# Performance work log

Hardware: AMD Instinct MI355X
Metric: run time of the kernel (lower is better)

The kernel has to match this reference:

```python
import jax, jax.numpy as jnp
import numpy as np

TOP_K = 2  # top-k experts per token


def setup_inputs() -> dict:
    key = jax.random.key(0)
    k1, k2, k3, k4, k5 = jax.random.split(key, 5)
    B, S, D = 1, 2048, 2048
    E, F = 8, 1408
    scale = 0.02
    return {
        "hidden_states": jax.random.normal(k1, (B, S, D), dtype=jnp.float32),
        "gate_w": jax.random.normal(k2, (E, D), dtype=jnp.float32) * scale,
        "w_gate": jax.random.normal(k3, (E, D, F), dtype=jnp.float32) * scale,
        "w_up": jax.random.normal(k4, (E, D, F), dtype=jnp.float32) * scale,
        "w_down": jax.random.normal(k5, (E, F, D), dtype=jnp.float32) * scale,
    }


def reference(hidden_states, gate_w, w_gate, w_up, w_down):
    B, S, D = hidden_states.shape
    T = B * S
    x = hidden_states.reshape(T, D)  # flatten tokens, as in forward()

    # Router: combined gate built from per-rank 1-row gates -> [T, E] logits
    router_logits = jnp.einsum("td,ed->te", x, gate_w)
    routing_weights = jax.nn.softmax(router_logits, axis=-1)
    top_w, top_idx = jax.lax.top_k(routing_weights, TOP_K)  # [T, K]

    # Per-token combine weight for each expert (0 if expert not selected).
    # Equivalent to the one_hot expert_mask + index_add combine in the module.
    comb = jnp.zeros((T, gate_w.shape[0]), dtype=routing_weights.dtype)
    comb = comb.at[jnp.arange(T)[:, None], top_idx].add(top_w)  # [T, E]

    # Each expert is a Qwen2 MLP: down(silu(gate(x)) * up(x)).
    # (Dispatch/all-to-all collapses to dense-per-expert + masked combine
    #  on a single device; tokens with comb==0 contribute nothing.)
    g = jnp.einsum("td,edf->etf", x, w_gate)
    u = jnp.einsum("td,edf->etf", x, w_up)
    y = jnp.einsum("etf,efd->etd", jax.nn.silu(g) * u, w_down)  # [E, T, D]

    out = jnp.einsum("te,etd->td", comb, y)  # weighted combine (index_add)
    return out.reshape(B, S, D)
```

## Files before the change

### kernel.cpp

```cpp
#include <hip/hip_runtime.h>
#include <stdint.h>


#define TT 2048
#define DD 2048
#define FF 1408
#define NE 8
#define HROWS 5120
#define TRASH (2*TT)

typedef float f32x4 __attribute__((ext_vector_type(4)));
typedef short bf16x8 __attribute__((ext_vector_type(8)));

__device__ __forceinline__ unsigned short f2bf(float f) {
    unsigned int x = __float_as_uint(f);
    return (unsigned short)((x + 0x7fffu + ((x >> 16) & 1u)) >> 16);
}
__device__ __forceinline__ float bf2f(unsigned short u) {
    union { unsigned int i; float f; } v; v.i = ((unsigned int)u) << 16; return v.f;
}
__device__ __forceinline__ uint4 cvt8(float4 a, float4 b) {
    uint4 o; unsigned short* po = (unsigned short*)&o;
    po[0] = f2bf(a.x); po[1] = f2bf(a.y); po[2] = f2bf(a.z); po[3] = f2bf(a.w);
    po[4] = f2bf(b.x); po[5] = f2bf(b.y); po[6] = f2bf(b.z); po[7] = f2bf(b.w);
    return o;
}

__device__ __forceinline__ void transpose_tile(const float* __restrict__ src,
                                               unsigned short* __restrict__ dst,
                                               int R, int C, int r0, int c0) {
    __shared__ unsigned short tile[64][65];
    const int tid = threadIdx.x;
    const int lr = tid >> 3;
    const int lc = (tid & 7) * 8;
#pragma unroll
    for (int p = 0; p < 2; ++p) {
        int rr = lr + p * 32;
        const float* sp = &src[(size_t)(r0 + rr) * C + c0 + lc];
        float4 a = ((const float4*)sp)[0];
        float4 b = ((const float4*)sp)[1];
        uint4 v = cvt8(a, b);
        const unsigned short* pv = (const unsigned short*)&v;
#pragma unroll
        for (int i = 0; i < 8; ++i) tile[rr][lc + i] = pv[i];
    }
    __syncthreads();
#pragma unroll
    for (int p = 0; p < 2; ++p) {
        int cc = lr + p * 32;
        uint4 o; unsigned short* po = (unsigned short*)&o;
#pragma unroll
        for (int i = 0; i < 8; ++i) po[i] = tile[lc + i][cc];
        *(uint4*)&dst[(size_t)(c0 + cc) * R + r0 + lc] = o;
    }
}

__global__ void transpose_gu_kernel(const float* __restrict__ wg,
                                    const float* __restrict__ wu,
                                    unsigned short* __restrict__ WgT,
                                    unsigned short* __restrict__ WuT) {
    const int z = blockIdx.z;
    const float* src; unsigned short* dst;
    if (z < 8) { src = wg + (size_t)z * DD * FF;       dst = WgT + (size_t)z * FF * DD; }
    else       { src = wu + (size_t)(z - 8) * DD * FF; dst = WuT + (size_t)(z - 8) * FF * DD; }
    transpose_tile(src, dst, DD, FF, blockIdx.y * 64, blockIdx.x * 64);
}

__global__ void transpose_d_kernel(const float* __restrict__ wd,
                                   unsigned short* __restrict__ WdT) {
    const int z = blockIdx.z;
    transpose_tile(wd + (size_t)z * FF * DD, WdT + (size_t)z * DD * FF,
                   FF, DD, blockIdx.y * 64, blockIdx.x * 64);
}

__global__ void router_kernel(const float* __restrict__ x,
                              const float* __restrict__ gw,
                              int* __restrict__ cnt,
                              int* __restrict__ tok,
                              float* __restrict__ wtv,
                              int* __restrict__ dstv) {
    const int wv = threadIdx.x >> 6, lane = threadIdx.x & 63;
    const int t = blockIdx.x * 4 + wv;
    float acc[NE];
#pragma unroll
    for (int e = 0; e < NE; ++e) acc[e] = 0.f;
    const float* xr = x + (size_t)t * DD;
    for (int j = lane; j < DD; j += 64) {
        float xv = xr[j];
#pragma unroll
        for (int e = 0; e < NE; ++e) acc[e] += xv * gw[e * DD + j];
    }
#pragma unroll
    for (int e = 0; e < NE; ++e) {
        float v = acc[e];
        v += __shfl_xor(v, 32); v += __shfl_xor(v, 16); v += __shfl_xor(v, 8);
        v += __shfl_xor(v, 4);  v += __shfl_xor(v, 2);  v += __shfl_xor(v, 1);
        acc[e] = v;
    }
    if (lane == 0) {
        float mx = acc[0];
#pragma unroll
        for (int e = 1; e < NE; ++e) mx = fmaxf(mx, acc[e]);
        float p[NE], s = 0.f;
#pragma unroll
        for (int e = 0; e < NE; ++e) { p[e] = __expf(acc[e] - mx); s += p[e]; }
        int i0 = 0;
#pragma unroll
        for (int e = 1; e < NE; ++e) if (p[e] > p[i0]) i0 = e;
        int i1 = (i0 == 0) ? 1 : 0;
#pragma unroll
        for (int e = 0; e < NE; ++e) if (e != i0 && p[e] > p[i1]) i1 = e;
        float inv = 1.f / s;
        int p0 = atomicAdd(&cnt[i0], 1);
        tok[i0 * TT + p0] = t; wtv[i0 * TT + p0] = p[i0] * inv; dstv[i0 * TT + p0] = 2 * t;
        int p1 = atomicAdd(&cnt[i1], 1);
        tok[i1 * TT + p1] = t; wtv[i1 * TT + p1] = p[i1] * inv; dstv[i1 * TT + p1] = 2 * t + 1;
    }
}

__global__ void finalize_kernel(const int* __restrict__ cnt,
                                int* __restrict__ base,
                                int* __restrict__ cntpad,
                                int* __restrict__ tok,
                                float* __restrict__ wtv,
                                int* __restrict__ dstv) {
    __shared__ int sc[NE], sp[NE];
    if (threadIdx.x == 0) {
        int b = 0;
        for (int e = 0; e < NE; ++e) {
            int c = cnt[e]; int pd = (c + 127) & ~127;
            base[e] = b; cntpad[e] = pd; sc[e] = c; sp[e] = pd; b += pd;
        }
    }
    __syncthreads();
    for (int e = 0; e < NE; ++e)
        for (int i = sc[e] + (int)threadIdx.x; i < sp[e]; i += 256) {
            tok[e * TT + i] = 0; wtv[e * TT + i] = 0.f; dstv[e * TT + i] = TRASH;
        }
}

__launch_bounds__(256, 2)
__global__ void gemm1_kernel(const float* __restrict__ x,
                             const unsigned short* __restrict__ WgT,
                             const unsigned short* __restrict__ WuT,
                             const int* __restrict__ tok,
                             const int* __restrict__ base,
                             const int* __restrict__ cntpad,
                             unsigned short* __restrict__ H) {
    __shared__ unsigned short As[128 * 32];
    __shared__ unsigned short Bg[128 * 32];
    __shared__ unsigned short Bu[128 * 32];
    __shared__ int s_tok[128];

    const int e = blockIdx.z, rb = blockIdx.y, fb = blockIdx.x;
    const int cp = cntpad[e];
    if (rb * 128 >= cp) return;
    const int b0 = base[e];

    const int tid = threadIdx.x;
    if (tid < 128) s_tok[tid] = tok[e * TT + rb * 128 + tid];
    __syncthreads();

    const int w = tid >> 6, lane = tid & 63;
    const int r = lane & 15, q = lane >> 4;
    const int wm = w & 1, wn = w >> 1;

    const int srow = w * 32 + (lane >> 2);
    const int koff = (lane & 3) * 8;
    const float* ga0 = x + (size_t)s_tok[srow] * DD + koff;
    const float* ga1 = x + (size_t)s_tok[srow + 16] * DD + koff;
    const size_t wb = (size_t)e * FF * DD + (size_t)(fb * 128 + srow) * DD + koff;
    const unsigned short* gg0 = WgT + wb;
    const unsigned short* gg1 = WgT + wb + (size_t)16 * DD;
    const unsigned short* gu0 = WuT + wb;
    const unsigned short* gu1 = WuT + wb + (size_t)16 * DD;
    uint4* sa0 = (uint4*)&As[srow * 32 + koff];  uint4* sa1 = (uint4*)&As[(srow + 16) * 32 + koff];
    uint4* sg0 = (uint4*)&Bg[srow * 32 + koff];  uint4* sg1 = (uint4*)&Bg[(srow + 16) * 32 + koff];
    uint4* su0 = (uint4*)&Bu[srow * 32 + koff];  uint4* su1 = (uint4*)&Bu[(srow + 16) * 32 + koff];

    f32x4 accg[4][4] = {};
    f32x4 accu[4][4] = {};

    for (int kt = 0; kt < DD / 32; ++kt) {
        uint4 va0 = cvt8(((const float4*)ga0)[0], ((const float4*)ga0)[1]);
        uint4 va1 = cvt8(((const float4*)ga1)[0], ((const float4*)ga1)[1]);
        uint4 vg0 = *(const uint4*)gg0;  uint4 vg1 = *(const uint4*)gg1;
        uint4 vu0 = *(const uint4*)gu0;  uint4 vu1 = *(const uint4*)gu1;
        ga0 += 32; ga1 += 32; gg0 += 32; gg1 += 32; gu0 += 32; gu1 += 32;
        __syncthreads();
        *sa0 = va0; *sa1 = va1; *sg0 = vg0; *sg1 = vg1; *su0 = vu0; *su1 = vu1;
        __syncthreads();
        bf16x8 af[4], gf[4], uf[4];
#pragma unroll
        for (int m = 0; m < 4; ++m)
            af[m] = *(const bf16x8*)&As[(wm * 64 + m * 16 + r) * 32 + q * 8];
#pragma unroll
        for (int n = 0; n < 4; ++n) {
            gf[n] = *(const bf16x8*)&Bg[(wn * 64 + n * 16 + r) * 32 + q * 8];
            uf[n] = *(const bf16x8*)&Bu[(wn * 64 + n * 16 + r) * 32 + q * 8];
        }
#pragma unroll
        for (int m = 0; m < 4; ++m)
#pragma unroll
            for (int n = 0; n < 4; ++n) {
                accg[m][n] = __builtin_amdgcn_mfma_f32_16x16x32_bf16(af[m], gf[n], accg[m][n], 0, 0, 0);
                accu[m][n] = __builtin_amdgcn_mfma_f32_16x16x32_bf16(af[m], uf[n], accu[m][n], 0, 0, 0);
            }
    }

    const size_t hr0 = (size_t)(b0 + rb * 128 + wm * 64);
#pragma unroll
    for (int m = 0; m < 4; ++m)
#pragma unroll
        for (int n = 0; n < 4; ++n)
#pragma unroll
            for (int rr = 0; rr < 4; ++rr) {
                float g = accg[m][n][rr], u = accu[m][n][rr];
                float h = (g / (1.f + __expf(-g))) * u;
                int row = m * 16 + q * 4 + rr;
                int col = fb * 128 + wn * 64 + n * 16 + r;
                H[(hr0 + row) * FF + col] = f2bf(h);
            }
}

__launch_bounds__(256, 2)
__global__ void gemm2_kernel(const unsigned short* __restrict__ H,
                             const unsigned short* __restrict__ WdT,
                             const float* __restrict__ wtv,
                             const int* __restrict__ dstv,
                             const int* __restrict__ base,
                             const int* __restrict__ cntpad,
                             unsigned short* __restrict__ Y) {
    __shared__ unsigned short As[128 * 32];
    __shared__ unsigned short Bs[128 * 32];
    __shared__ float s_w[128];
    __shared__ int s_d[128];

    const int e = blockIdx.z, rb = blockIdx.y, db = blockIdx.x;
    const int cp = cntpad[e];
    if (rb * 128 >= cp) return;
    const int b0 = base[e];

    const int tid = threadIdx.x;
    if (tid < 128) {
        int idx = e * TT + rb * 128 + tid;
        s_w[tid] = wtv[idx]; s_d[tid] = dstv[idx];
    }
    __syncthreads();

    const int w = tid >> 6, lane = tid & 63;
    const int r = lane & 15, q = lane >> 4;
    const int wm = w & 1, wn = w >> 1;

    const int srow = w * 32 + (lane >> 2);
    const int koff = (lane & 3) * 8;
    const unsigned short* ga0 = H + (size_t)(b0 + rb * 128 + srow) * FF + koff;
    const unsigned short* ga1 = ga0 + (size_t)16 * FF;
    const unsigned short* gb0 = WdT + (size_t)e * DD * FF + (size_t)(db * 128 + srow) * FF + koff;
    const unsigned short* gb1 = gb0 + (size_t)16 * FF;
    uint4* sa0 = (uint4*)&As[srow * 32 + koff];  uint4* sa1 = (uint4*)&As[(srow + 16) * 32 + koff];
    uint4* sb0 = (uint4*)&Bs[srow * 32 + koff];  uint4* sb1 = (uint4*)&Bs[(srow + 16) * 32 + koff];

    f32x4 acc[4][4] = {};

    for (int kt = 0; kt < FF / 32; ++kt) {
        uint4 va0 = *(const uint4*)ga0;  uint4 va1 = *(const uint4*)ga1;
        uint4 vb0 = *(const uint4*)gb0;  uint4 vb1 = *(const uint4*)gb1;
        ga0 += 32; ga1 += 32; gb0 += 32; gb1 += 32;
        __syncthreads();
        *sa0 = va0; *sa1 = va1; *sb0 = vb0; *sb1 = vb1;
        __syncthreads();
        bf16x8 af[4], bf[4];
#pragma unroll
        for (int m = 0; m < 4; ++m)
            af[m] = *(const bf16x8*)&As[(wm * 64 + m * 16 + r) * 32 + q * 8];
#pragma unroll
        for (int n = 0; n < 4; ++n)
            bf[n] = *(const bf16x8*)&Bs[(wn * 64 + n * 16 + r) * 32 + q * 8];
#pragma unroll
        for (int m = 0; m < 4; ++m)
#pragma unroll
            for (int n = 0; n < 4; ++n)
                acc[m][n] = __builtin_amdgcn_mfma_f32_16x16x32_bf16(af[m], bf[n], acc[m][n], 0, 0, 0);
    }

#pragma unroll
    for (int m = 0; m < 4; ++m)
#pragma unroll
        for (int n = 0; n < 4; ++n)
#pragma unroll
            for (int rr = 0; rr < 4; ++rr) {
                int row = wm * 64 + m * 16 + q * 4 + rr;
                int col = db * 128 + wn * 64 + n * 16 + r;
                float v = s_w[row] * acc[m][n][rr];
                Y[(size_t)s_d[row] * DD + col] = f2bf(v);
            }
}

__global__ void combine_kernel(const unsigned short* __restrict__ Y,
                               float* __restrict__ out) {
    const int t = blockIdx.x;
    const int d = threadIdx.x * 8;
    uint4 a = *(const uint4*)(Y + (size_t)(2 * t) * DD + d);
    uint4 b = *(const uint4*)(Y + (size_t)(2 * t + 1) * DD + d);
    const unsigned short* pa = (const unsigned short*)&a;
    const unsigned short* pb = (const unsigned short*)&b;
    float4 o0, o1;
    o0.x = bf2f(pa[0]) + bf2f(pb[0]);  o0.y = bf2f(pa[1]) + bf2f(pb[1]);
    o0.z = bf2f(pa[2]) + bf2f(pb[2]);  o0.w = bf2f(pa[3]) + bf2f(pb[3]);
    o1.x = bf2f(pa[4]) + bf2f(pb[4]);  o1.y = bf2f(pa[5]) + bf2f(pb[5]);
    o1.z = bf2f(pa[6]) + bf2f(pb[6]);  o1.w = bf2f(pa[7]) + bf2f(pb[7]);
    float* op = out + (size_t)t * DD + d;
    ((float4*)op)[0] = o0;
    ((float4*)op)[1] = o1;
}

extern "C" void kernel_launch(void* const* d_in, const int* in_sizes, int n_in,
                              void* d_out, int out_size, void* d_ws, size_t ws_size,
                              hipStream_t stream) {
    const float* x      = (const float*)d_in[0];
    const float* gw     = (const float*)d_in[1];
    const float* w_gate = (const float*)d_in[2];
    const float* w_up   = (const float*)d_in[3];
    const float* w_down = (const float*)d_in[4];
    float* out = (float*)d_out;

    uint8_t* ws = (uint8_t*)d_ws;
    size_t off = 0;
    auto alloc = [&](size_t bytes) -> void* {
        void* p = ws + off;
        off = (off + bytes + 255) & ~(size_t)255;
        return p;
    };
    int*   cnt    = (int*)  alloc(NE * 4);
    int*   basep  = (int*)  alloc(NE * 4);
    int*   cntpad = (int*)  alloc(NE * 4);
    int*   tok    = (int*)  alloc((size_t)NE * TT * 4);
    float* wtv    = (float*)alloc((size_t)NE * TT * 4);
    int*   dstv   = (int*)  alloc((size_t)NE * TT * 4);
    unsigned short* Hb  = (unsigned short*)alloc((size_t)HROWS * FF * 2);
    unsigned short* Yb  = (unsigned short*)alloc((size_t)(2 * TT + 8) * DD * 2);
    unsigned short* WT  = (unsigned short*)alloc((size_t)2 * NE * FF * DD * 2);
    unsigned short* WgT = WT;
    unsigned short* WuT = WT + (size_t)NE * FF * DD;
    unsigned short* WdT = WT;
    (void)ws_size; (void)in_sizes; (void)n_in; (void)out_size;

    hipMemsetAsync(cnt, 0, NE * 4, stream);
    transpose_gu_kernel<<<dim3(22, 32, 16), 256, 0, stream>>>(w_gate, w_up, WgT, WuT);
    router_kernel<<<dim3(TT / 4), 256, 0, stream>>>(x, gw, cnt, tok, wtv, dstv);
    finalize_kernel<<<1, 256, 0, stream>>>(cnt, basep, cntpad, tok, wtv, dstv);
    gemm1_kernel<<<dim3(FF / 128, TT / 128, NE), 256, 0, stream>>>(x, WgT, WuT, tok, basep, cntpad, Hb);
    transpose_d_kernel<<<dim3(32, 22, 8), 256, 0, stream>>>(w_down, WdT);
    gemm2_kernel<<<dim3(DD / 128, TT / 128, NE), 256, 0, stream>>>(Hb, WdT, wtv, dstv, basep, cntpad, Yb);
    combine_kernel<<<dim3(TT), 256, 0, stream>>>(Yb, out);
}
```

Baseline: 517.2 us.

## Pre-convert activations to bf16 and stream GEMM tiles via direct global-to-LDS loads

Adds a kernel that converts x to bf16 once, so gemm1 no longer repeats the fp32-to-bf16 conversion on every K step. Both expert GEMMs now use global_load_lds 16-byte copies straight into shared memory instead of staging through registers, which removes one barrier-separated store phase per iteration. The N tile is halved from 128 to 64, doubling the grid and cutting accumulator registers. The trade-off is less weight and activation reuse per block, an extra conversion pass over x, and reliance on correct wait handling for the async LDS loads.

```diff
diff --git a/kernel.cpp b/kernel.cpp
--- a/kernel.cpp
+++ b/kernel.cpp
@@ -24,6 +24,18 @@
     po[0] = f2bf(a.x); po[1] = f2bf(a.y); po[2] = f2bf(a.z); po[3] = f2bf(a.w);
     po[4] = f2bf(b.x); po[5] = f2bf(b.y); po[6] = f2bf(b.z); po[7] = f2bf(b.w);
     return o;
+}
+__device__ __forceinline__ void gld16(const void* g, void* l) {
+    __builtin_amdgcn_global_load_lds((const __attribute__((address_space(1))) void*)g,
+                                     (__attribute__((address_space(3))) void*)l, 16, 0, 0);
+}
+
+__global__ void convert_x_kernel(const float* __restrict__ x,
+                                 unsigned short* __restrict__ xb) {
+    const size_t i = ((size_t)blockIdx.x * 256 + threadIdx.x) * 8;
+    float4 a = ((const float4*)(x + i))[0];
+    float4 b = ((const float4*)(x + i))[1];
+    *(uint4*)(xb + i) = cvt8(a, b);
 }
 
 __device__ __forceinline__ void transpose_tile(const float* __restrict__ src,
@@ -140,7 +152,7 @@
 }
 
 __launch_bounds__(256, 2)
-__global__ void gemm1_kernel(const float* __restrict__ x,
+__global__ void gemm1_kernel(const unsigned short* __restrict__ Xb,
                              const unsigned short* __restrict__ WgT,
                              const unsigned short* __restrict__ WuT,
                              const int* __restrict__ tok,
@@ -148,8 +160,8 @@
                              const int* __restrict__ cntpad,
                              unsigned short* __restrict__ H) {
     __shared__ unsigned short As[128 * 32];
-    __shared__ unsigned short Bg[128 * 32];
-    __shared__ unsigned short Bu[128 * 32];
+    __shared__ unsigned short Bg[64 * 32];
+    __shared__ unsigned short Bu[64 * 32];
     __shared__ int s_tok[128];
 
     const int e = blockIdx.z, rb = blockIdx.y, fb = blockIdx.x;
@@ -165,60 +177,57 @@
     const int r = lane & 15, q = lane >> 4;
     const int wm = w & 1, wn = w >> 1;
 
-    const int srow = w * 32 + (lane >> 2);
+    const int arow = w * 32 + (lane >> 2);
+    const int brow = w * 16 + (lane >> 2);
     const int koff = (lane & 3) * 8;
-    const float* ga0 = x + (size_t)s_tok[srow] * DD + koff;
-    const float* ga1 = x + (size_t)s_tok[srow + 16] * DD + koff;
-    const size_t wb = (size_t)e * FF * DD + (size_t)(fb * 128 + srow) * DD + koff;
-    const unsigned short* gg0 = WgT + wb;
-    const unsigned short* gg1 = WgT + wb + (size_t)16 * DD;
-    const unsigned short* gu0 = WuT + wb;
-    const unsigned short* gu1 = WuT + wb + (size_t)16 * DD;
-    uint4* sa0 = (uint4*)&As[srow * 32 + koff];  uint4* sa1 = (uint4*)&As[(srow + 16) * 32 + koff];
-    uint4* sg0 = (uint4*)&Bg[srow * 32 + koff];  uint4* sg1 = (uint4*)&Bg[(srow + 16) * 32 + koff];
-    uint4* su0 = (uint4*)&Bu[srow * 32 + koff];  uint4* su1 = (uint4*)&Bu[(srow + 16) * 32 + koff];
-
-    f32x4 accg[4][4] = {};
-    f32x4 accu[4][4] = {};
+    const unsigned short* ga0 = Xb + (size_t)s_tok[arow] * DD + koff;
+    const unsigned short* ga1 = Xb + (size_t)s_tok[arow + 16] * DD + koff;
+    const size_t wb = (size_t)e * FF * DD + (size_t)(fb * 64 + brow) * DD + koff;
+    const unsigned short* gg = WgT + wb;
+    const unsigned short* gu = WuT + wb;
+    unsigned short* la0 = As + arow * 32 + koff;
+    unsigned short* la1 = la0 + 16 * 32;
+    unsigned short* lg  = Bg + brow * 32 + koff;
+    unsigned short* lu  = Bu + brow * 32 + koff;
+
+    f32x4 accg[4][2] = {};
+    f32x4 accu[4][2] = {};
 
     for (int kt = 0; kt < DD / 32; ++kt) {
-        uint4 va0 = cvt8(((const float4*)ga0)[0], ((const float4*)ga0)[1]);
-        uint4 va1 = cvt8(((const float4*)ga1)[0], ((const float4*)ga1)[1]);
-        uint4 vg0 = *(const uint4*)gg0;  uint4 vg1 = *(const uint4*)gg1;
-        uint4 vu0 = *(const uint4*)gu0;  uint4 vu1 = *(const uint4*)gu1;
-        ga0 += 32; ga1 += 32; gg0 += 32; gg1 += 32; gu0 += 32; gu1 += 32;
+        gld16(ga0, la0); gld16(ga1, la1);
+        gld16(gg, lg);   gld16(gu, lu);
+        ga0 += 32; ga1 += 32; gg += 32; gu += 32;
         __syncthreads();
-        *sa0 = va0; *sa1 = va1; *sg0 = vg0; *sg1 = vg1; *su0 = vu0; *su1 = vu1;
-        __syncthreads();
-        bf16x8 af[4], gf[4], uf[4];
+        bf16x8 af[4], gf[2], uf[2];
 #pragma unroll
         for (int m = 0; m < 4; ++m)
             af[m] = *(const bf16x8*)&As[(wm * 64 + m * 16 + r) * 32 + q * 8];
 #pragma unroll
-        for (int n = 0; n < 4; ++n) {
-            gf[n] = *(const bf16x8*)&Bg[(wn * 64 + n * 16 + r) * 32 + q * 8];
-            uf[n] = *(const bf16x8*)&Bu[(wn * 64 + n * 16 + r) * 32 + q * 8];
+        for (int n = 0; n < 2; ++n) {
+            gf[n] = *(const bf16x8*)&Bg[(wn * 32 + n * 16 + r) * 32 + q * 8];
+            uf[n] = *(const bf16x8*)&Bu[(wn * 32 + n * 16 + r) * 32 + q * 8];
         }
 #pragma unroll
         for (int m = 0; m < 4; ++m)
 #pragma unroll
-            for (int n = 0; n < 4; ++n) {
+            for (int n = 0; n < 2; ++n) {
                 accg[m][n] = __builtin_amdgcn_mfma_f32_16x16x32_bf16(af[m], gf[n], accg[m][n], 0, 0, 0);
                 accu[m][n] = __builtin_amdgcn_mfma_f32_16x16x32_bf16(af[m], uf[n], accu[m][n], 0, 0, 0);
             }
+        __syncthreads();
     }
 
     const size_t hr0 = (size_t)(b0 + rb * 128 + wm * 64);
 #pragma unroll
     for (int m = 0; m < 4; ++m)
 #pragma unroll
-        for (int n = 0; n < 4; ++n)
+        for (int n = 0; n < 2; ++n)
 #pragma unroll
             for (int rr = 0; rr < 4; ++rr) {
                 float g = accg[m][n][rr], u = accu[m][n][rr];
                 float h = (g / (1.f + __expf(-g))) * u;
                 int row = m * 16 + q * 4 + rr;
-                int col = fb * 128 + wn * 64 + n * 16 + r;
+                int col = fb * 64 + wn * 32 + n * 16 + r;
                 H[(hr0 + row) * FF + col] = f2bf(h);
             }
 }
@@ -232,7 +241,7 @@
                              const int* __restrict__ cntpad,
                              unsigned short* __restrict__ Y) {
     __shared__ unsigned short As[128 * 32];
-    __shared__ unsigned short Bs[128 * 32];
+    __shared__ unsigned short Bs[64 * 32];
     __shared__ float s_w[128];
     __shared__ int s_d[128];
 
@@ -252,46 +261,45 @@
     const int r = lane & 15, q = lane >> 4;
     const int wm = w & 1, wn = w >> 1;
 
-    const int srow = w * 32 + (lane >> 2);
+    const int arow = w * 32 + (lane >> 2);
+    const int brow = w * 16 + (lane >> 2);
     const int koff = (lane & 3) * 8;
-    const unsigned short* ga0 = H + (size_t)(b0 + rb * 128 + srow) * FF + koff;
+    const unsigned short* ga0 = H + (size_t)(b0 + rb * 128 + arow) * FF + koff;
     const unsigned short* ga1 = ga0 + (size_t)16 * FF;
-    const unsigned short* gb0 = WdT + (size_t)e * DD * FF + (size_t)(db * 128 + srow) * FF + koff;
-    const unsigned short* gb1 = gb0 + (size_t)16 * FF;
-    uint4* sa0 = (uint4*)&As[srow * 32 + koff];  uint4* sa1 = (uint4*)&As[(srow + 16) * 32 + koff];
-    uint4* sb0 = (uint4*)&Bs[srow * 32 + koff];  uint4* sb1 = (uint4*)&Bs[(srow + 16) * 32 + koff];
-
-    f32x4 acc[4][4] = {};
+    const unsigned short* gb = WdT + (size_t)e * DD * FF + (size_t)(db * 64 + brow) * FF + koff;
+    unsigned short* la0 = As + arow * 32 + koff;
+    unsigned short* la1 = la0 + 16 * 32;
+    unsigned short* lb  = Bs + brow * 32 + koff;
+
+    f32x4 acc[4][2] = {};
 
     for (int kt = 0; kt < FF / 32; ++kt) {
-        uint4 va0 = *(const uint4*)ga0;  uint4 va1 = *(const uint4*)ga1;
-        uint4 vb0 = *(const uint4*)gb0;  uint4 vb1 = *(const uint4*)gb1;
-        ga0 += 32; ga1 += 32; gb0 += 32; gb1 += 32;
+        gld16(ga0, la0); gld16(ga1, la1); gld16(gb, lb);
+        ga0 += 32; ga1 += 32; gb += 32;
         __syncthreads();
-        *sa0 = va0; *sa1 = va1; *sb0 = vb0; *sb1 = vb1;
-        __syncthreads();
-        bf16x8 af[4], bf[4];
+        bf16x8 af[4], bf[2];
 #pragma unroll
         for (int m = 0; m < 4; ++m)
             af[m] = *(const bf16x8*)&As[(wm * 64 + m * 16 + r) * 32 + q * 8];
 #pragma unroll
-        for (int n = 0; n < 4; ++n)
-            bf[n] = *(const bf16x8*)&Bs[(wn * 64 + n * 16 + r) * 32 + q * 8];
+        for (int n = 0; n < 2; ++n)
+            bf[n] = *(const bf16x8*)&Bs[(wn * 32 + n * 16 + r) * 32 + q * 8];
 #pragma unroll
         for (int m = 0; m < 4; ++m)
 #pragma unroll
-            for (int n = 0; n < 4; ++n)
+            for (int n = 0; n < 2; ++n)
                 acc[m][n] = __builtin_amdgcn_mfma_f32_16x16x32_bf16(af[m], bf[n], acc[m][n], 0, 0, 0);
+        __syncthreads();
     }
 
 #pragma unroll
     for (int m = 0; m < 4; ++m)
 #pragma unroll
-        for (int n = 0; n < 4; ++n)
+        for (int n = 0; n < 2; ++n)
 #pragma unroll
             for (int rr = 0; rr < 4; ++rr) {
                 int row = wm * 64 + m * 16 + q * 4 + rr;
-                int col = db * 128 + wn * 64 + n * 16 + r;
+                int col = db * 64 + wn * 32 + n * 16 + r;
                 float v = s_w[row] * acc[m][n][rr];
                 Y[(size_t)s_d[row] * DD + col] = f2bf(v);
             }
@@ -338,6 +346,7 @@
     int*   tok    = (int*)  alloc((size_t)NE * TT * 4);
     float* wtv    = (float*)alloc((size_t)NE * TT * 4);
     int*   dstv   = (int*)  alloc((size_t)NE * TT * 4);
+    unsigned short* Xb  = (unsigned short*)alloc((size_t)TT * DD * 2);
     unsigned short* Hb  = (unsigned short*)alloc((size_t)HROWS * FF * 2);
     unsigned short* Yb  = (unsigned short*)alloc((size_t)(2 * TT + 8) * DD * 2);
     unsigned short* WT  = (unsigned short*)alloc((size_t)2 * NE * FF * DD * 2);
@@ -347,11 +356,12 @@
     (void)ws_size; (void)in_sizes; (void)n_in; (void)out_size;
 
     hipMemsetAsync(cnt, 0, NE * 4, stream);
+    convert_x_kernel<<<dim3(TT * DD / 2048), 256, 0, stream>>>(x, Xb);
     transpose_gu_kernel<<<dim3(22, 32, 16), 256, 0, stream>>>(w_gate, w_up, WgT, WuT);
     router_kernel<<<dim3(TT / 4), 256, 0, stream>>>(x, gw, cnt, tok, wtv, dstv);
     finalize_kernel<<<1, 256, 0, stream>>>(cnt, basep, cntpad, tok, wtv, dstv);
-    gemm1_kernel<<<dim3(FF / 128, TT / 128, NE), 256, 0, stream>>>(x, WgT, WuT, tok, basep, cntpad, Hb);
+    gemm1_kernel<<<dim3(FF / 64, TT / 128, NE), 256, 0, stream>>>(Xb, WgT, WuT, tok, basep, cntpad, Hb);
     transpose_d_kernel<<<dim3(32, 22, 8), 256, 0, stream>>>(w_down, WdT);
-    gemm2_kernel<<<dim3(DD / 128, TT / 128, NE), 256, 0, stream>>>(Hb, WdT, wtv, dstv, basep, cntpad, Yb);
+    gemm2_kernel<<<dim3(DD / 64, TT / 128, NE), 256, 0, stream>>>(Hb, WdT, wtv, dstv, basep, cntpad, Yb);
     combine_kernel<<<dim3(TT), 256, 0, stream>>>(Yb, out);
 }
```

Measured after the change: 528.9 us. +2.3%, slower.
